# Optimization experiments

Hardware: AMD Instinct MI355X
Metric: run time of the kernel (lower is better)

Reference implementation:

```python
import jax, jax.numpy as jnp
import numpy as np
import math

DEPTH = 6
D_MODEL = 512
N_HEADS = 8
D_HEAD = D_MODEL // N_HEADS
D_FF = 2048
SEQ_LEN = 2048
VOCAB = 256
B, T = 2, 2048
EPS = 1e-5


def setup_inputs() -> dict:
    key = jax.random.key(0)
    ks = jax.random.split(key, 16)
    std = 0.02
    std_proj = 0.02 / math.sqrt(2 * DEPTH)
    inp = {
        "x": jax.random.randint(ks[0], (B, T), 0, VOCAB, dtype=jnp.int64)
             if jax.config.jax_enable_x64 else
             jax.random.randint(ks[0], (B, T), 0, VOCAB, dtype=jnp.int32),
        "tok_emb": std * jax.random.normal(ks[1], (VOCAB, D_MODEL), jnp.float32),
        "pos_emb": std * jax.random.normal(ks[2], (SEQ_LEN, D_MODEL), jnp.float32),
        "qkv_w": std * jax.random.normal(ks[3], (DEPTH, 3 * D_MODEL, D_MODEL), jnp.float32),
        "proj_w": std_proj * jax.random.normal(ks[4], (DEPTH, D_MODEL, D_MODEL), jnp.float32),
        "ln1_w": jnp.ones((DEPTH, D_MODEL), jnp.float32),
        "ln1_b": jnp.zeros((DEPTH, D_MODEL), jnp.float32),
        "ln2_w": jnp.ones((DEPTH, D_MODEL), jnp.float32),
        "ln2_b": jnp.zeros((DEPTH, D_MODEL), jnp.float32),
        "fc1_w": std * jax.random.normal(ks[5], (DEPTH, D_FF, D_MODEL), jnp.float32),
        "fc2_w": std_proj * jax.random.normal(ks[6], (DEPTH, D_MODEL, D_FF), jnp.float32),
        "lnf_w": jnp.ones((D_MODEL,), jnp.float32),
        "lnf_b": jnp.zeros((D_MODEL,), jnp.float32),
        "head_w": std * jax.random.normal(ks[7], (VOCAB, D_MODEL), jnp.float32),
    }
    return inp


def _layernorm(x, w, b):
    mu = jnp.mean(x, axis=-1, keepdims=True)
    var = jnp.mean(jnp.square(x - mu), axis=-1, keepdims=True)
    return (x - mu) * jax.lax.rsqrt(var + EPS) * w + b


def _attention(x, qkv_w, proj_w):
    Bq, Tq, d = x.shape
    qkv = jnp.einsum('btd,ed->bte', x, qkv_w)  # [B,T,3d]
    q, k, v = jnp.split(qkv, 3, axis=-1)
    def split(t):
        return t.reshape(Bq, Tq, N_HEADS, D_HEAD).transpose(0, 2, 1, 3)  # [B,H,T,Dh]
    q, k, v = split(q), split(k), split(v)
    scores = jnp.einsum('bhqd,bhkd->bhqk', q, k) / math.sqrt(D_HEAD)
    mask = jnp.tril(jnp.ones((Tq, Tq), dtype=bool))
    scores = jnp.where(mask, scores, -jnp.inf)
    attn = jax.nn.softmax(scores, axis=-1)
    out = jnp.einsum('bhqk,bhkd->bhqd', attn, v)
    out = out.transpose(0, 2, 1, 3).reshape(Bq, Tq, d)
    return jnp.einsum('btd,ed->bte', out, proj_w)


def reference(x, tok_emb, pos_emb, qkv_w, proj_w, ln1_w, ln1_b, ln2_w, ln2_b,
              fc1_w, fc2_w, lnf_w, lnf_b, head_w):
    Tq = x.shape[1]
    h = tok_emb[x] + pos_emb[:Tq][None, :, :]  # [B,T,d]
    for l in range(DEPTH):
        a = _attention(_layernorm(h, ln1_w[l], ln1_b[l]), qkv_w[l], proj_w[l])
        h = h + a
        m = _layernorm(h, ln2_w[l], ln2_b[l])
        m = jax.nn.gelu(jnp.einsum('btd,fd->btf', m, fc1_w[l]), approximate=False)
        h = h + jnp.einsum('btf,df->btd', m, fc2_w[l])
    h = _layernorm(h, lnf_w, lnf_b)
    return jnp.einsum('btd,vd->btv', h, head_w)  # [B,T,VOCAB]
```

## Files before the change

### kernel.cpp

```cpp
#include <hip/hip_runtime.h>
#include <hip/hip_bf16.h>
#include <math.h>

typedef __hip_bfloat16 bf16;
typedef __attribute__((ext_vector_type(8))) short short8;
typedef __attribute__((ext_vector_type(4))) float f32x4;

#define DEPTH 6
#define DM    512
#define NH    8
#define DH    64
#define DFF   2048
#define TSEQ  2048
#define BATCH 2
#define ROWS  (BATCH*TSEQ)
#define NVOCAB 256

#define GLDS(gp, lp) __builtin_amdgcn_global_load_lds( \
    (const __attribute__((address_space(1))) void*)(gp), \
    (__attribute__((address_space(3))) void*)(lp), 16, 0, 0)

__device__ __forceinline__ short f2bs(float x) {
    union { bf16 b; short s; } u; u.b = __float2bfloat16(x); return u.s;
}

__global__ __launch_bounds__(256) void w2b_kernel(const float* __restrict__ s,
    bf16* __restrict__ d)
{
    size_t i = ((size_t)blockIdx.x * 256 + threadIdx.x) * 8;
    float4 f0 = *(const float4*)(s + i);
    float4 f1 = *(const float4*)(s + i + 4);
    short8 p;
    p[0] = f2bs(f0.x); p[1] = f2bs(f0.y); p[2] = f2bs(f0.z); p[3] = f2bs(f0.w);
    p[4] = f2bs(f1.x); p[5] = f2bs(f1.y); p[6] = f2bs(f1.z); p[7] = f2bs(f1.w);
    *(short8*)((short*)d + i) = p;
}

__global__ __launch_bounds__(256) void emb_kernel(const int* __restrict__ x,
    const float* __restrict__ tok, const float* __restrict__ pos, float* __restrict__ h)
{
    int i = blockIdx.x * 256 + threadIdx.x;
    int d = i & (DM - 1);
    int r = i >> 9;
    int t = r & (TSEQ - 1);
    h[i] = tok[x[r] * DM + d] + pos[t * DM + d];
}

__global__ __launch_bounds__(256) void ln_kernel(const float* __restrict__ x,
    const float* __restrict__ w, const float* __restrict__ b, bf16* __restrict__ out)
{
    int row = blockIdx.x * 4 + (threadIdx.x >> 6);
    int lane = threadIdx.x & 63;
    const float* xr = x + (size_t)row * DM;

    float4 v0 = *(const float4*)(xr + lane * 4);
    float4 v1 = *(const float4*)(xr + 256 + lane * 4);

    float s = v0.x + v0.y + v0.z + v0.w + v1.x + v1.y + v1.z + v1.w;
    #pragma unroll
    for (int m = 1; m < 64; m <<= 1) s += __shfl_xor(s, m, 64);
    float mu = s * (1.f / DM);

    float var = (v0.x-mu)*(v0.x-mu) + (v0.y-mu)*(v0.y-mu) + (v0.z-mu)*(v0.z-mu)
              + (v0.w-mu)*(v0.w-mu) + (v1.x-mu)*(v1.x-mu) + (v1.y-mu)*(v1.y-mu)
              + (v1.z-mu)*(v1.z-mu) + (v1.w-mu)*(v1.w-mu);
    #pragma unroll
    for (int m = 1; m < 64; m <<= 1) var += __shfl_xor(var, m, 64);
    float rstd = rsqrtf(var * (1.f / DM) + 1e-5f);

    float4 w0 = *(const float4*)(w + lane * 4);
    float4 w1 = *(const float4*)(w + 256 + lane * 4);
    float4 b0 = *(const float4*)(b + lane * 4);
    float4 b1 = *(const float4*)(b + 256 + lane * 4);

    short4 o0, o1;
    o0.x = f2bs((v0.x - mu) * rstd * w0.x + b0.x);
    o0.y = f2bs((v0.y - mu) * rstd * w0.y + b0.y);
    o0.z = f2bs((v0.z - mu) * rstd * w0.z + b0.z);
    o0.w = f2bs((v0.w - mu) * rstd * w0.w + b0.w);
    o1.x = f2bs((v1.x - mu) * rstd * w1.x + b1.x);
    o1.y = f2bs((v1.y - mu) * rstd * w1.y + b1.y);
    o1.z = f2bs((v1.z - mu) * rstd * w1.z + b1.z);
    o1.w = f2bs((v1.w - mu) * rstd * w1.w + b1.w);
    *(short4*)(out + (size_t)row * DM + lane * 4) = o0;
    *(short4*)(out + (size_t)row * DM + 256 + lane * 4) = o1;
}

template<int EPI, typename WT>
__global__ __launch_bounds__(256) void mfma_gemm(const bf16* __restrict__ A,
    const WT* __restrict__ W, void* __restrict__ Cv, int M, int N, int K)
{
    __shared__ short As[128 * 32];
    __shared__ short Bs[128 * 32];
    int tid = threadIdx.x;
    int bm0 = blockIdx.y * 128, bn0 = blockIdx.x * 128;
    int lane = tid & 63, w = tid >> 6;
    int wr = (w >> 1) * 64, wc = (w & 1) * 64;
    int fr = lane & 15, fk = (lane >> 4) * 8;

    f32x4 acc[4][4] = {};

    for (int k0 = 0; k0 < K; k0 += 32) {
        #pragma unroll
        for (int it = 0; it < 2; it++) {
            int c = it * 256 + tid;
            int row = c >> 2, kc = (c & 3) * 8;
            GLDS((const short*)A + (size_t)(bm0 + row) * K + k0 + kc, &As[c * 8]);
        }
        if constexpr (sizeof(WT) == 2) {
            #pragma unroll
            for (int it = 0; it < 2; it++) {
                int c = it * 256 + tid;
                int row = c >> 2, kc = (c & 3) * 8;
                GLDS((const short*)W + (size_t)(bn0 + row) * K + k0 + kc, &Bs[c * 8]);
            }
        } else {
            #pragma unroll
            for (int it = 0; it < 2; it++) {
                int c = it * 256 + tid;
                int row = c >> 2, kc = (c & 3) * 8;
                const float* wp = (const float*)W + (size_t)(bn0 + row) * K + k0 + kc;
                float4 f0 = *(const float4*)wp;
                float4 f1 = *(const float4*)(wp + 4);
                short8 p;
                p[0] = f2bs(f0.x); p[1] = f2bs(f0.y); p[2] = f2bs(f0.z); p[3] = f2bs(f0.w);
                p[4] = f2bs(f1.x); p[5] = f2bs(f1.y); p[6] = f2bs(f1.z); p[7] = f2bs(f1.w);
                *(short8*)&Bs[c * 8] = p;
            }
        }
        __syncthreads();

        short8 af[4], bfr[4];
        #pragma unroll
        for (int i = 0; i < 4; i++)
            af[i] = *(short8*)&As[(wr + i * 16 + fr) * 32 + fk];
        #pragma unroll
        for (int j = 0; j < 4; j++)
            bfr[j] = *(short8*)&Bs[(wc + j * 16 + fr) * 32 + fk];
        #pragma unroll
        for (int i = 0; i < 4; i++)
            #pragma unroll
            for (int j = 0; j < 4; j++)
                acc[i][j] = __builtin_amdgcn_mfma_f32_16x16x32_bf16(
                    af[i], bfr[j], acc[i][j], 0, 0, 0);
        __syncthreads();
    }

    int cr = (lane >> 4) * 4, cc = lane & 15;
    #pragma unroll
    for (int i = 0; i < 4; i++)
        #pragma unroll
        for (int j = 0; j < 4; j++)
            #pragma unroll
            for (int r = 0; r < 4; r++) {
                int m = bm0 + wr + i * 16 + cr + r;
                int n = bn0 + wc + j * 16 + cc;
                size_t o = (size_t)m * N + n;
                float v = acc[i][j][r];
                if (EPI == 0)      ((bf16*)Cv)[o] = __float2bfloat16(v);
                else if (EPI == 1) ((float*)Cv)[o] += v;
                else if (EPI == 2) ((bf16*)Cv)[o] =
                    __float2bfloat16(0.5f * v * (1.0f + erff(v * 0.70710678118654752f)));
                else               ((float*)Cv)[o] = v;
            }
}

template<int EPI, typename WT>
__global__ __launch_bounds__(256) void mfma_gemm_n64(const bf16* __restrict__ A,
    const WT* __restrict__ W, void* __restrict__ Cv, int M, int N, int K, int ldb)
{
    __shared__ short As[128 * 32];
    __shared__ short Bs[64 * 32];
    int tid = threadIdx.x;
    int bm0 = blockIdx.y * 128, bn0 = blockIdx.x * 64;
    int lane = tid & 63, w = tid >> 6;
    int wm = (w & 1) * 64, wn = (w >> 1) * 32;
    int fr = lane & 15, fk = (lane >> 4) * 8;

    f32x4 acc[4][2] = {};

    for (int k0 = 0; k0 < K; k0 += 32) {
        #pragma unroll
        for (int it = 0; it < 2; it++) {
            int c = it * 256 + tid;
            int row = c >> 2, kc = (c & 3) * 8;
            GLDS((const short*)A + (size_t)(bm0 + row) * K + k0 + kc, &As[c * 8]);
        }
        if constexpr (sizeof(WT) == 2) {
            int c = tid;
            int row = c >> 2, kc = (c & 3) * 8;
            GLDS((const short*)W + (size_t)(bn0 + row) * ldb + k0 + kc, &Bs[c * 8]);
        } else {
            int row = tid >> 2, kc = (tid & 3) * 8;
            const float* wp = (const float*)W + (size_t)(bn0 + row) * ldb + k0 + kc;
            float4 f0 = *(const float4*)wp;
            float4 f1 = *(const float4*)(wp + 4);
            short8 p;
            p[0] = f2bs(f0.x); p[1] = f2bs(f0.y); p[2] = f2bs(f0.z); p[3] = f2bs(f0.w);
            p[4] = f2bs(f1.x); p[5] = f2bs(f1.y); p[6] = f2bs(f1.z); p[7] = f2bs(f1.w);
            *(short8*)&Bs[tid * 8] = p;
        }
        __syncthreads();

        short8 af[4], bfr[2];
        #pragma unroll
        for (int i = 0; i < 4; i++)
            af[i] = *(short8*)&As[(wm + i * 16 + fr) * 32 + fk];
        #pragma unroll
        for (int j = 0; j < 2; j++)
            bfr[j] = *(short8*)&Bs[(wn + j * 16 + fr) * 32 + fk];
        #pragma unroll
        for (int i = 0; i < 4; i++)
            #pragma unroll
            for (int j = 0; j < 2; j++)
                acc[i][j] = __builtin_amdgcn_mfma_f32_16x16x32_bf16(
                    af[i], bfr[j], acc[i][j], 0, 0, 0);
        __syncthreads();
    }

    int cr = (lane >> 4) * 4, cc = lane & 15;
    #pragma unroll
    for (int i = 0; i < 4; i++)
        #pragma unroll
        for (int j = 0; j < 2; j++)
            #pragma unroll
            for (int r = 0; r < 4; r++) {
                int m = bm0 + wm + i * 16 + cr + r;
                int n = bn0 + wn + j * 16 + cc;
                size_t o = (size_t)m * N + n;
                float v = acc[i][j][r];
                if (EPI == 0)      ((bf16*)Cv)[o] = __float2bfloat16(v);
                else if (EPI == 1) ((float*)Cv)[o] += v;
                else if (EPI == 2) ((bf16*)Cv)[o] =
                    __float2bfloat16(0.5f * v * (1.0f + erff(v * 0.70710678118654752f)));
                else               ((float*)Cv)[o] = v;
            }
}

__device__ __forceinline__ int swz(int row, int sh) {
    return row * 72 + ((((sh >> 3) + (row >> 3)) & 7) << 3) + (sh & 7);
}
__device__ __forceinline__ int pswz(int row, int col) {
    return row * 136 + ((((col >> 3) + row) & 15) << 3) + (col & 7);
}

__global__ __launch_bounds__(256) void fattn_kernel(const bf16* __restrict__ qkv,
    bf16* __restrict__ out)
{
    __shared__ short Ks[128 * 72];
    __shared__ short Vt[64 * 136];
    __shared__ short Ps[4][16 * 136];

    int tid = threadIdx.x;
    int lane = tid & 63, w = tid >> 6;
    int quad = lane >> 4, cl = lane & 15;
    int qt = (TSEQ / 64 - 1) - blockIdx.x;
    int bh = blockIdx.y;
    int b = bh >> 3, hd = bh & 7;
    int q0 = qt * 64;
    const size_t rstr = 3 * DM;
    const bf16* base = qkv + (size_t)b * TSEQ * rstr;
    short* Pw = &Ps[w][0];

    short8 qf[2];
    {
        const bf16* qrow = base + (size_t)(q0 + w * 16 + cl) * rstr + hd * DH;
        qf[0] = *(const short8*)(qrow + quad * 8);
        qf[1] = *(const short8*)(qrow + 32 + quad * 8);
    }

    float l_r[4] = {0.f, 0.f, 0.f, 0.f};
    f32x4 o_acc[4] = {};

    int nkt = (q0 + 64 + 127) >> 7;
    int skey = tid & 127, sc0 = (tid >> 7) * 4;

    for (int kt = 0; kt < nkt; kt++) {
        int k0 = kt * 128;
        __syncthreads();
        {
            const bf16* krow = base + (size_t)(k0 + skey) * rstr + DM + hd * DH;
            const bf16* vrow = krow + DM;
            #pragma unroll
            for (int it = 0; it < 4; it++) {
                int c = sc0 + it;
                short8 kv = *(const short8*)(krow + c * 8);
                *(short8*)&Ks[swz(skey, c * 8)] = kv;
                short8 vv = *(const short8*)(vrow + c * 8);
                #pragma unroll
                for (int e = 0; e < 8; e++)
                    Vt[pswz(c * 8 + e, skey)] = vv[e];
            }
        }
        __syncthreads();

        f32x4 s[8];
        #pragma unroll
        for (int j = 0; j < 8; j++) {
            short8 kf0 = *(short8*)&Ks[swz(j * 16 + cl, quad * 8)];
            short8 kf1 = *(short8*)&Ks[swz(j * 16 + cl, 32 + quad * 8)];
            f32x4 a = {};
            a = __builtin_amdgcn_mfma_f32_16x16x32_bf16(qf[0], kf0, a, 0, 0, 0);
            a = __builtin_amdgcn_mfma_f32_16x16x32_bf16(qf[1], kf1, a, 0, 0, 0);
            s[j] = a;
        }

        int grow = q0 + w * 16 + quad * 4;
        bool last = (kt == nkt - 1);
        #pragma unroll
        for (int j = 0; j < 8; j++)
            #pragma unroll
            for (int r = 0; r < 4; r++) {
                bool masked = last && (k0 + j * 16 + cl) > (grow + r);
                float p = masked ? 0.f : __expf(s[j][r] * 0.125f);
                s[j][r] = p;
                l_r[r] += p;
            }

        #pragma unroll
        for (int j = 0; j < 8; j++)
            #pragma unroll
            for (int r = 0; r < 4; r++)
                Pw[pswz(quad * 4 + r, j * 16 + cl)] = f2bs(s[j][r]);
        short8 pf[4];
        #pragma unroll
        for (int c = 0; c < 4; c++)
            pf[c] = *(short8*)&Pw[pswz(cl, c * 32 + quad * 8)];

        #pragma unroll
        for (int j = 0; j < 4; j++)
            #pragma unroll
            for (int c = 0; c < 4; c++) {
                short8 vf = *(short8*)&Vt[pswz(j * 16 + cl, c * 32 + quad * 8)];
                o_acc[j] = __builtin_amdgcn_mfma_f32_16x16x32_bf16(
                    pf[c], vf, o_acc[j], 0, 0, 0);
            }
    }

    int grow = q0 + w * 16 + quad * 4;
    #pragma unroll
    for (int r = 0; r < 4; r++) {
        float l = l_r[r];
        #pragma unroll
        for (int m = 1; m < 16; m <<= 1) l += __shfl_xor(l, m, 64);
        float inv = 1.f / l;
        #pragma unroll
        for (int j = 0; j < 4; j++)
            out[(size_t)(b * TSEQ + grow + r) * DM + hd * DH + j * 16 + cl] =
                __float2bfloat16(o_acc[j][r] * inv);
    }
}

template<typename WT>
static void run_model(const int* x, const float* tok, const float* pos,
    const WT* qkvw, const WT* projw,
    const float* ln1w, const float* ln1b, const float* ln2w, const float* ln2b,
    const WT* fc1w, const WT* fc2w, const float* lnfw, const float* lnfb,
    const WT* headw, float* h, bf16* xn, bf16* q3, float* dout, hipStream_t stream)
{
    emb_kernel<<<ROWS * DM / 256, 256, 0, stream>>>(x, tok, pos, h);

    for (int l = 0; l < DEPTH; l++) {
        ln_kernel<<<ROWS / 4, 256, 0, stream>>>(h, ln1w + l * DM, ln1b + l * DM, xn);
        mfma_gemm<0, WT><<<dim3(3 * DM / 128, ROWS / 128), 256, 0, stream>>>(
            xn, qkvw + (size_t)l * 3 * DM * DM, q3, ROWS, 3 * DM, DM);
        fattn_kernel<<<dim3(TSEQ / 64, BATCH * NH), 256, 0, stream>>>(q3, xn);
        mfma_gemm_n64<1, WT><<<dim3(DM / 64, ROWS / 128), 256, 0, stream>>>(
            xn, projw + (size_t)l * DM * DM, h, ROWS, DM, DM, DM);
        ln_kernel<<<ROWS / 4, 256, 0, stream>>>(h, ln2w + l * DM, ln2b + l * DM, xn);
        for (int p = 0; p < 2; p++) {
            mfma_gemm<2, WT><<<dim3(1024 / 128, ROWS / 128), 256, 0, stream>>>(
                xn, fc1w + (size_t)l * DFF * DM + (size_t)p * 1024 * DM,
                q3, ROWS, 1024, DM);
            mfma_gemm_n64<1, WT><<<dim3(DM / 64, ROWS / 128), 256, 0, stream>>>(
                q3, fc2w + (size_t)l * DM * DFF + (size_t)p * 1024,
                h, ROWS, DM, 1024, DFF);
        }
    }

    ln_kernel<<<ROWS / 4, 256, 0, stream>>>(h, lnfw, lnfb, xn);
    mfma_gemm_n64<3, WT><<<dim3(NVOCAB / 64, ROWS / 128), 256, 0, stream>>>(
        xn, headw, dout, ROWS, NVOCAB, DM, DM);
}

extern "C" void kernel_launch(void* const* d_in, const int* in_sizes, int n_in,
                              void* d_out, int out_size, void* d_ws, size_t ws_size,
                              hipStream_t stream)
{
    const int*   x     = (const int*)d_in[0];
    const float* tok   = (const float*)d_in[1];
    const float* pos   = (const float*)d_in[2];
    const float* qkvw  = (const float*)d_in[3];
    const float* projw = (const float*)d_in[4];
    const float* ln1w  = (const float*)d_in[5];
    const float* ln1b  = (const float*)d_in[6];
    const float* ln2w  = (const float*)d_in[7];
    const float* ln2b  = (const float*)d_in[8];
    const float* fc1w  = (const float*)d_in[9];
    const float* fc2w  = (const float*)d_in[10];
    const float* lnfw  = (const float*)d_in[11];
    const float* lnfb  = (const float*)d_in[12];
    const float* headw = (const float*)d_in[13];

    char* ws = (char*)d_ws;
    float* h  = (float*)ws;
    bf16*  xn = (bf16*)(ws + (8u << 20));
    bf16*  q3 = (bf16*)(ws + (12u << 20));

    constexpr size_t SZ_QKV  = (size_t)DEPTH * 3 * DM * DM;
    constexpr size_t SZ_PROJ = (size_t)DEPTH * DM * DM;
    constexpr size_t SZ_FC1  = (size_t)DEPTH * DFF * DM;
    constexpr size_t SZ_FC2  = SZ_FC1;
    constexpr size_t SZ_HEAD = (size_t)NVOCAB * DM;
    constexpr size_t SZ_ALL  = SZ_QKV + SZ_PROJ + SZ_FC1 + SZ_FC2 + SZ_HEAD;
    const size_t need = ((size_t)24 << 20) + 2 * SZ_ALL;

    if (ws_size >= need) {
        bf16* qkvwb  = (bf16*)(ws + (24u << 20));
        bf16* projwb = qkvwb + SZ_QKV;
        bf16* fc1wb  = projwb + SZ_PROJ;
        bf16* fc2wb  = fc1wb + SZ_FC1;
        bf16* headwb = fc2wb + SZ_FC2;
        w2b_kernel<<<SZ_QKV  / 2048, 256, 0, stream>>>(qkvw,  qkvwb);
        w2b_kernel<<<SZ_PROJ / 2048, 256, 0, stream>>>(projw, projwb);
        w2b_kernel<<<SZ_FC1  / 2048, 256, 0, stream>>>(fc1w,  fc1wb);
        w2b_kernel<<<SZ_FC2  / 2048, 256, 0, stream>>>(fc2w,  fc2wb);
        w2b_kernel<<<SZ_HEAD / 2048, 256, 0, stream>>>(headw, headwb);
        run_model<bf16>(x, tok, pos, qkvwb, projwb, ln1w, ln1b, ln2w, ln2b,
                        fc1wb, fc2wb, lnfw, lnfb, headwb,
                        h, xn, q3, (float*)d_out, stream);
    } else {
        run_model<float>(x, tok, pos, qkvw, projw, ln1w, ln1b, ln2w, ln2b,
                         fc1w, fc2w, lnfw, lnfb, headw,
                         h, xn, q3, (float*)d_out, stream);
    }
}
```

Measured before the change: 1.339 ms.

## Write Q, K and transposed V in attention-friendly layouts from QKV GEMM epilogue

The QKV GEMM gets a new epilogue that scatters Q and K into separate contiguous buffers and writes V already transposed per (batch, head). The attention kernel can then load K and V tiles straight into LDS with global_load_lds and XOR-style chunk swizzles, instead of register loads plus a scalar per-element V transpose. The five weight-conversion launches are also merged into one kernel. The transposed V stores in the GEMM epilogue are strided and scattered, which may cost write efficiency there.

Result: slower. 1.422 ms (+6.2%).

```diff
diff --git a/kernel.cpp b/kernel.cpp
--- a/kernel.cpp
+++ b/kernel.cpp
@@ -16,6 +16,16 @@
 #define ROWS  (BATCH*TSEQ)
 #define NVOCAB 256
 
+#define Q3_K_OFF  2097152
+#define Q3_VT_OFF 4194304
+
+constexpr size_t SZ_QKV  = (size_t)DEPTH * 3 * DM * DM;
+constexpr size_t SZ_PROJ = (size_t)DEPTH * DM * DM;
+constexpr size_t SZ_FC1  = (size_t)DEPTH * DFF * DM;
+constexpr size_t SZ_FC2  = SZ_FC1;
+constexpr size_t SZ_HEAD = (size_t)NVOCAB * DM;
+constexpr size_t SZ_ALL  = SZ_QKV + SZ_PROJ + SZ_FC1 + SZ_FC2 + SZ_HEAD;
+
 #define GLDS(gp, lp) __builtin_amdgcn_global_load_lds( \
     (const __attribute__((address_space(1))) void*)(gp), \
     (__attribute__((address_space(3))) void*)(lp), 16, 0, 0)
@@ -24,16 +34,23 @@
     union { bf16 b; short s; } u; u.b = __float2bfloat16(x); return u.s;
 }
 
-__global__ __launch_bounds__(256) void w2b_kernel(const float* __restrict__ s,
-    bf16* __restrict__ d)
+__global__ __launch_bounds__(256) void w2b_all(const float* __restrict__ q,
+    const float* __restrict__ p, const float* __restrict__ f1,
+    const float* __restrict__ f2, const float* __restrict__ hw, bf16* __restrict__ dst)
 {
     size_t i = ((size_t)blockIdx.x * 256 + threadIdx.x) * 8;
-    float4 f0 = *(const float4*)(s + i);
-    float4 f1 = *(const float4*)(s + i + 4);
-    short8 p;
-    p[0] = f2bs(f0.x); p[1] = f2bs(f0.y); p[2] = f2bs(f0.z); p[3] = f2bs(f0.w);
-    p[4] = f2bs(f1.x); p[5] = f2bs(f1.y); p[6] = f2bs(f1.z); p[7] = f2bs(f1.w);
-    *(short8*)((short*)d + i) = p;
+    const float* s; size_t off;
+    if      (i < SZ_QKV)                               { s = q;  off = 0; }
+    else if (i < SZ_QKV + SZ_PROJ)                     { s = p;  off = SZ_QKV; }
+    else if (i < SZ_QKV + SZ_PROJ + SZ_FC1)            { s = f1; off = SZ_QKV + SZ_PROJ; }
+    else if (i < SZ_QKV + SZ_PROJ + SZ_FC1 + SZ_FC2)   { s = f2; off = SZ_QKV + SZ_PROJ + SZ_FC1; }
+    else                                               { s = hw; off = SZ_QKV + SZ_PROJ + SZ_FC1 + SZ_FC2; }
+    float4 f0 = *(const float4*)(s + (i - off));
+    float4 f1v = *(const float4*)(s + (i - off) + 4);
+    short8 o;
+    o[0] = f2bs(f0.x); o[1] = f2bs(f0.y); o[2] = f2bs(f0.z); o[3] = f2bs(f0.w);
+    o[4] = f2bs(f1v.x); o[5] = f2bs(f1v.y); o[6] = f2bs(f1v.z); o[7] = f2bs(f1v.w);
+    *(short8*)((short*)dst + i) = o;
 }
 
 __global__ __launch_bounds__(256) void emb_kernel(const int* __restrict__ x,
@@ -155,13 +172,27 @@
             for (int r = 0; r < 4; r++) {
                 int m = bm0 + wr + i * 16 + cr + r;
                 int n = bn0 + wc + j * 16 + cc;
-                size_t o = (size_t)m * N + n;
                 float v = acc[i][j][r];
-                if (EPI == 0)      ((bf16*)Cv)[o] = __float2bfloat16(v);
-                else if (EPI == 1) ((float*)Cv)[o] += v;
-                else if (EPI == 2) ((bf16*)Cv)[o] =
-                    __float2bfloat16(0.5f * v * (1.0f + erff(v * 0.70710678118654752f)));
-                else               ((float*)Cv)[o] = v;
+                if (EPI == 4) {
+                    short* q3s = (short*)Cv;
+                    short sv = f2bs(v);
+                    if (n < 512)
+                        q3s[(size_t)m * 512 + n] = sv;
+                    else if (n < 1024)
+                        q3s[Q3_K_OFF + (size_t)m * 512 + (n - 512)] = sv;
+                    else {
+                        int bb = m >> 11, key = m & 2047;
+                        int hd = (n - 1024) >> 6, dim = (n - 1024) & 63;
+                        q3s[Q3_VT_OFF + (((size_t)(bb * 8 + hd) * 64 + dim) << 11) + key] = sv;
+                    }
+                } else {
+                    size_t o = (size_t)m * N + n;
+                    if (EPI == 0)      ((bf16*)Cv)[o] = __float2bfloat16(v);
+                    else if (EPI == 1) ((float*)Cv)[o] += v;
+                    else if (EPI == 2) ((bf16*)Cv)[o] =
+                        __float2bfloat16(0.5f * v * (1.0f + erff(v * 0.70710678118654752f)));
+                    else               ((float*)Cv)[o] = v;
+                }
             }
 }
 
@@ -187,9 +218,8 @@
             GLDS((const short*)A + (size_t)(bm0 + row) * K + k0 + kc, &As[c * 8]);
         }
         if constexpr (sizeof(WT) == 2) {
-            int c = tid;
-            int row = c >> 2, kc = (c & 3) * 8;
-            GLDS((const short*)W + (size_t)(bn0 + row) * ldb + k0 + kc, &Bs[c * 8]);
+            int row = tid >> 2, kc = (tid & 3) * 8;
+            GLDS((const short*)W + (size_t)(bn0 + row) * ldb + k0 + kc, &Bs[tid * 8]);
         } else {
             int row = tid >> 2, kc = (tid & 3) * 8;
             const float* wp = (const float*)W + (size_t)(bn0 + row) * ldb + k0 + kc;
@@ -237,19 +267,12 @@
             }
 }
 
-__device__ __forceinline__ int swz(int row, int sh) {
-    return row * 72 + ((((sh >> 3) + (row >> 3)) & 7) << 3) + (sh & 7);
-}
-__device__ __forceinline__ int pswz(int row, int col) {
-    return row * 136 + ((((col >> 3) + row) & 15) << 3) + (col & 7);
-}
-
-__global__ __launch_bounds__(256) void fattn_kernel(const bf16* __restrict__ qkv,
+__global__ __launch_bounds__(256) void fattn_kernel(const short* __restrict__ q3,
     bf16* __restrict__ out)
 {
-    __shared__ short Ks[128 * 72];
-    __shared__ short Vt[64 * 136];
-    __shared__ short Ps[4][16 * 136];
+    __shared__ __align__(16) short Ks[128 * 64];
+    __shared__ __align__(16) short Vt[64 * 128];
+    __shared__ __align__(16) short Ps[4][16 * 128];
 
     int tid = threadIdx.x;
     int lane = tid & 63, w = tid >> 6;
@@ -258,13 +281,14 @@
     int bh = blockIdx.y;
     int b = bh >> 3, hd = bh & 7;
     int q0 = qt * 64;
-    const size_t rstr = 3 * DM;
-    const bf16* base = qkv + (size_t)b * TSEQ * rstr;
+    const short* Qb = q3;
+    const short* Kb = q3 + Q3_K_OFF;
+    const short* Vb = q3 + Q3_VT_OFF + (size_t)bh * 64 * 2048;
     short* Pw = &Ps[w][0];
 
     short8 qf[2];
     {
-        const bf16* qrow = base + (size_t)(q0 + w * 16 + cl) * rstr + hd * DH;
+        const short* qrow = Qb + (size_t)(b * 2048 + q0 + w * 16 + cl) * 512 + hd * 64;
         qf[0] = *(const short8*)(qrow + quad * 8);
         qf[1] = *(const short8*)(qrow + 32 + quad * 8);
     }
@@ -273,32 +297,33 @@
     f32x4 o_acc[4] = {};
 
     int nkt = (q0 + 64 + 127) >> 7;
-    int skey = tid & 127, sc0 = (tid >> 7) * 4;
 
     for (int kt = 0; kt < nkt; kt++) {
         int k0 = kt * 128;
         __syncthreads();
-        {
-            const bf16* krow = base + (size_t)(k0 + skey) * rstr + DM + hd * DH;
-            const bf16* vrow = krow + DM;
-            #pragma unroll
-            for (int it = 0; it < 4; it++) {
-                int c = sc0 + it;
-                short8 kv = *(const short8*)(krow + c * 8);
-                *(short8*)&Ks[swz(skey, c * 8)] = kv;
-                short8 vv = *(const short8*)(vrow + c * 8);
-                #pragma unroll
-                for (int e = 0; e < 8; e++)
-                    Vt[pswz(c * 8 + e, skey)] = vv[e];
-            }
+        #pragma unroll
+        for (int it = 0; it < 4; it++) {
+            int slot = it * 256 + tid;
+            int key = slot >> 3, pc = slot & 7;
+            int chunk = (pc - key) & 7;
+            GLDS(Kb + (size_t)(b * 2048 + k0 + key) * 512 + hd * 64 + chunk * 8,
+                 &Ks[slot * 8]);
+        }
+        #pragma unroll
+        for (int it = 0; it < 4; it++) {
+            int slot = it * 256 + tid;
+            int dim = slot >> 4, pc = slot & 15;
+            int chunk = (pc - dim) & 15;
+            GLDS(Vb + (size_t)dim * 2048 + k0 + chunk * 8, &Vt[slot * 8]);
         }
         __syncthreads();
 
         f32x4 s[8];
         #pragma unroll
         for (int j = 0; j < 8; j++) {
-            short8 kf0 = *(short8*)&Ks[swz(j * 16 + cl, quad * 8)];
-            short8 kf1 = *(short8*)&Ks[swz(j * 16 + cl, 32 + quad * 8)];
+            int key = j * 16 + cl;
+            short8 kf0 = *(short8*)&Ks[key * 64 + ((quad + key) & 7) * 8];
+            short8 kf1 = *(short8*)&Ks[key * 64 + ((4 + quad + key) & 7) * 8];
             f32x4 a = {};
             a = __builtin_amdgcn_mfma_f32_16x16x32_bf16(qf[0], kf0, a, 0, 0, 0);
             a = __builtin_amdgcn_mfma_f32_16x16x32_bf16(qf[1], kf1, a, 0, 0, 0);
@@ -318,20 +343,26 @@
             }
 
         #pragma unroll
-        for (int j = 0; j < 8; j++)
-            #pragma unroll
-            for (int r = 0; r < 4; r++)
-                Pw[pswz(quad * 4 + r, j * 16 + cl)] = f2bs(s[j][r]);
+        for (int j = 0; j < 8; j++) {
+            int key = j * 16 + cl;
+            int kc = key >> 3;
+            #pragma unroll
+            for (int r = 0; r < 4; r++) {
+                int row = quad * 4 + r;
+                Pw[row * 128 + ((kc + row) & 15) * 8 + (key & 7)] = f2bs(s[j][r]);
+            }
+        }
         short8 pf[4];
         #pragma unroll
         for (int c = 0; c < 4; c++)
-            pf[c] = *(short8*)&Pw[pswz(cl, c * 32 + quad * 8)];
+            pf[c] = *(short8*)&Pw[cl * 128 + ((c * 4 + quad + cl) & 15) * 8];
 
         #pragma unroll
         for (int j = 0; j < 4; j++)
             #pragma unroll
             for (int c = 0; c < 4; c++) {
-                short8 vf = *(short8*)&Vt[pswz(j * 16 + cl, c * 32 + quad * 8)];
+                int dim = j * 16 + cl;
+                short8 vf = *(short8*)&Vt[dim * 128 + ((c * 4 + quad + dim) & 15) * 8];
                 o_acc[j] = __builtin_amdgcn_mfma_f32_16x16x32_bf16(
                     pf[c], vf, o_acc[j], 0, 0, 0);
             }
@@ -362,9 +393,9 @@
 
     for (int l = 0; l < DEPTH; l++) {
         ln_kernel<<<ROWS / 4, 256, 0, stream>>>(h, ln1w + l * DM, ln1b + l * DM, xn);
-        mfma_gemm<0, WT><<<dim3(3 * DM / 128, ROWS / 128), 256, 0, stream>>>(
+        mfma_gemm<4, WT><<<dim3(3 * DM / 128, ROWS / 128), 256, 0, stream>>>(
             xn, qkvw + (size_t)l * 3 * DM * DM, q3, ROWS, 3 * DM, DM);
-        fattn_kernel<<<dim3(TSEQ / 64, BATCH * NH), 256, 0, stream>>>(q3, xn);
+        fattn_kernel<<<dim3(TSEQ / 64, BATCH * NH), 256, 0, stream>>>((short*)q3, xn);
         mfma_gemm_n64<1, WT><<<dim3(DM / 64, ROWS / 128), 256, 0, stream>>>(
             xn, projw + (size_t)l * DM * DM, h, ROWS, DM, DM, DM);
         ln_kernel<<<ROWS / 4, 256, 0, stream>>>(h, ln2w + l * DM, ln2b + l * DM, xn);
@@ -407,25 +438,16 @@
     bf16*  xn = (bf16*)(ws + (8u << 20));
     bf16*  q3 = (bf16*)(ws + (12u << 20));
 
-    constexpr size_t SZ_QKV  = (size_t)DEPTH * 3 * DM * DM;
-    constexpr size_t SZ_PROJ = (size_t)DEPTH * DM * DM;
-    constexpr size_t SZ_FC1  = (size_t)DEPTH * DFF * DM;
-    constexpr size_t SZ_FC2  = SZ_FC1;
-    constexpr size_t SZ_HEAD = (size_t)NVOCAB * DM;
-    constexpr size_t SZ_ALL  = SZ_QKV + SZ_PROJ + SZ_FC1 + SZ_FC2 + SZ_HEAD;
     const size_t need = ((size_t)24 << 20) + 2 * SZ_ALL;
 
     if (ws_size >= need) {
-        bf16* qkvwb  = (bf16*)(ws + (24u << 20));
-        bf16* projwb = qkvwb + SZ_QKV;
-        bf16* fc1wb  = projwb + SZ_PROJ;
-        bf16* fc2wb  = fc1wb + SZ_FC1;
-        bf16* headwb = fc2wb + SZ_FC2;
-        w2b_kernel<<<SZ_QKV  / 2048, 256, 0, stream>>>(qkvw,  qkvwb);
-        w2b_kernel<<<SZ_PROJ / 2048, 256, 0, stream>>>(projw, projwb);
-        w2b_kernel<<<SZ_FC1  / 2048, 256, 0, stream>>>(fc1w,  fc1wb);
-        w2b_kernel<<<SZ_FC2  / 2048, 256, 0, stream>>>(fc2w,  fc2wb);
-        w2b_kernel<<<SZ_HEAD / 2048, 256, 0, stream>>>(headw, headwb);
+        bf16* wb = (bf16*)(ws + (24u << 20));
+        w2b_all<<<SZ_ALL / 2048, 256, 0, stream>>>(qkvw, projw, fc1w, fc2w, headw, wb);
+        const bf16* qkvwb  = wb;
+        const bf16* projwb = qkvwb + SZ_QKV;
+        const bf16* fc1wb  = projwb + SZ_PROJ;
+        const bf16* fc2wb  = fc1wb + SZ_FC1;
+        const bf16* headwb = fc2wb + SZ_FC2;
         run_model<bf16>(x, tok, pos, qkvwb, projwb, ln1w, ln1b, ln2w, ln2b,
                         fc1wb, fc2wb, lnfw, lnfb, headwb,
                         h, xn, q3, (float*)d_out, stream);
```
